# Performance work log

Measured on AMD Instinct MI355X. Metric: run time of the kernel, lower is better.

## Reference

```python
import jax, jax.numpy as jnp
import numpy as np

S, DIM, E, K = 16384, 4096, 64, 2

def setup_inputs() -> dict:
    key = jax.random.key(0)
    kx, kw = jax.random.split(key)
    x = jax.random.normal(kx, (S, DIM), dtype=jnp.float32)
    W = jax.random.normal(kw, (E, DIM), dtype=jnp.float32) * (1.0 / np.sqrt(DIM))
    b = jnp.zeros((E,), dtype=jnp.float32)
    return {"x": x, "W": W, "b": b}

def reference(x, W, b):
    # Router linear: [S, dim] @ [dim, E] + [E] -> [S, E]
    logits = jnp.einsum('sd,ed->se', x, W) + b
    probs = jax.nn.softmax(logits, axis=-1)              # [S, E]
    topk_vals, topk_idx = jax.lax.top_k(probs, K)        # [S, K], [S, K]
    # Load-balance aux loss (Switch Transformer style)
    importance = probs.mean(axis=0)                      # [E]
    hard1 = topk_idx[:, 0]                               # [S]
    load = jax.ops.segment_sum(jnp.ones((S,), dtype=probs.dtype), hard1,
                               num_segments=E) / max(S, 1)
    aux_loss = E * jnp.sum(importance * load)
    return (topk_idx, topk_vals, aux_loss)
```

## Files before the change

### kernel.cpp

```cpp
#include <hip/hip_runtime.h>
#include <hip/hip_bf16.h>

#define SROWS 16384
#define DIMK  4096
#define NE    64
#define BM    16
#define NBLK  (SROWS/BM)
#define KSEG  1024
#define NSTEP 16
#define WSPLIT_SHORTS 262144
#define WSOFF_F 262144
#define WSOFF2  (WSOFF_F + NBLK*64)

typedef __attribute__((ext_vector_type(8))) short short8;
typedef __attribute__((ext_vector_type(4))) float f32x4;

__device__ __forceinline__ void split8(const float4 a, const float4 c, short8& hi, short8& lo) {
    float f[8] = {a.x, a.y, a.z, a.w, c.x, c.y, c.z, c.w};
    #pragma unroll
    for (int i = 0; i < 8; ++i) {
        unsigned short h = __bfloat16_as_ushort(__float2bfloat16(f[i]));
        float hf = __uint_as_float((unsigned)h << 16);
        unsigned short l = __bfloat16_as_ushort(__float2bfloat16(f[i] - hf));
        hi[i] = (short)h;
        lo[i] = (short)l;
    }
}

__global__ void w_split(const float* __restrict__ W, unsigned short* __restrict__ wsp)
{
    const int idx   = blockIdx.x * 256 + threadIdx.x;
    const int kslot = idx & 511;
    const int e     = idx >> 9;
    const float* p = W + (size_t)e * DIMK + kslot * 8;
    float4 va = *reinterpret_cast<const float4*>(p);
    float4 vb = *reinterpret_cast<const float4*>(p + 4);
    short8 hi, lo;
    split8(va, vb, hi, lo);
    *reinterpret_cast<short8*>(wsp + (size_t)(kslot * 64 + e) * 8)                 = hi;
    *reinterpret_cast<short8*>(wsp + WSPLIT_SHORTS + (size_t)(kslot * 64 + e) * 8) = lo;
}

__global__ __launch_bounds__(256, 4) void gate_main(
    const float* __restrict__ x, const unsigned short* __restrict__ wsp,
    const float* __restrict__ b, float* __restrict__ out, float* __restrict__ ws)
{
    __shared__ float smem[4672];
    float* const part = smem;
    float* const Lb   = smem + 3072;
    float* const red  = smem + 4160;

    const int tid  = threadIdx.x;
    const int lane = tid & 63;
    const int ksw  = __builtin_amdgcn_readfirstlane(tid >> 6);
    const int row0 = blockIdx.x * BM;

    const float* xA = x + (size_t)(row0 + (lane & 15)) * DIMK
                        + ksw * KSEG + (lane >> 4) * 8;
    const unsigned short* wBbase = wsp + ((size_t)(ksw * 128) * 64) * 8;

    f32x4 acc[4];
    #pragma unroll
    for (int n = 0; n < 4; ++n) acc[n] = (f32x4){0.f, 0.f, 0.f, 0.f};

    float4 a00 = *reinterpret_cast<const float4*>(xA);
    float4 a01 = *reinterpret_cast<const float4*>(xA + 4);
    float4 a10 = *reinterpret_cast<const float4*>(xA + 32);
    float4 a11 = *reinterpret_cast<const float4*>(xA + 36);

    #pragma unroll 1
    for (int st = 0; st < NSTEP; ++st) {
        const int pst = (st + 1 < NSTEP) ? st + 1 : NSTEP - 1;
        const float* xp = xA + (size_t)pst * 64;
        float4 p00 = *reinterpret_cast<const float4*>(xp);
        float4 p01 = *reinterpret_cast<const float4*>(xp + 4);
        float4 p10 = *reinterpret_cast<const float4*>(xp + 32);
        float4 p11 = *reinterpret_cast<const float4*>(xp + 36);
        __builtin_amdgcn_sched_barrier(0);

        #pragma unroll
        for (int c2 = 0; c2 < 2; ++c2) {
            short8 ah, al;
            if (c2 == 0) split8(a00, a01, ah, al);
            else         split8(a10, a11, ah, al);

            const int ksl = st * 8 + c2 * 4 + (lane >> 4);
            const unsigned short* bp = wBbase + ((size_t)ksl * 64 + (lane & 15)) * 8;
            short8 bh[4], bl[4];
            #pragma unroll
            for (int n = 0; n < 4; ++n) {
                bh[n] = *reinterpret_cast<const short8*>(bp + n * 128);
                bl[n] = *reinterpret_cast<const short8*>(bp + WSPLIT_SHORTS + n * 128);
            }

            #pragma unroll
            for (int n = 0; n < 4; ++n)
                acc[n] = __builtin_amdgcn_mfma_f32_16x16x32_bf16(ah, bh[n], acc[n], 0, 0, 0);
            #pragma unroll
            for (int n = 0; n < 4; ++n)
                acc[n] = __builtin_amdgcn_mfma_f32_16x16x32_bf16(ah, bl[n], acc[n], 0, 0, 0);
            #pragma unroll
            for (int n = 0; n < 4; ++n)
                acc[n] = __builtin_amdgcn_mfma_f32_16x16x32_bf16(al, bh[n], acc[n], 0, 0, 0);
        }

        __builtin_amdgcn_sched_barrier(0);
        a00 = p00; a01 = p01; a10 = p10; a11 = p11;
    }

    __syncthreads();

    if (ksw > 0) {
        #pragma unroll
        for (int n = 0; n < 4; ++n)
            #pragma unroll
            for (int j = 0; j < 4; ++j)
                part[(ksw - 1) * 1024 + lane * 16 + n * 4 + j] = acc[n][j];
    }
    __syncthreads();
    if (ksw == 0) {
        #pragma unroll
        for (int n = 0; n < 4; ++n) {
            #pragma unroll
            for (int j = 0; j < 4; ++j) {
                float v = acc[n][j]
                        + part[0 * 1024 + lane * 16 + n * 4 + j]
                        + part[1 * 1024 + lane * 16 + n * 4 + j]
                        + part[2 * 1024 + lane * 16 + n * 4 + j];
                const int e  = n * 16 + (lane & 15);
                const int rl = (lane >> 4) * 4 + j;
                Lb[e * 17 + rl] = v;
            }
        }
    }
    __syncthreads();

    float impAcc = 0.f, cntAcc = 0.f;
    const float blane = b[lane];
    float* outIdx = out;
    float* outVal = out + (size_t)SROWS * 2;

    #pragma unroll 1
    for (int rr = 0; rr < 4; ++rr) {
        const int r = ksw * 4 + rr;
        const float logit = Lb[lane * 17 + r] + blane;

        float v1 = logit; int i1 = lane;
        #pragma unroll
        for (int off = 32; off; off >>= 1) {
            float ov = __shfl_xor(v1, off);
            int   oi = __shfl_xor(i1, off);
            if (ov > v1 || (ov == v1 && oi < i1)) { v1 = ov; i1 = oi; }
        }
        float p = expf(logit - v1);
        float ssum = p;
        #pragma unroll
        for (int off = 32; off; off >>= 1) ssum += __shfl_xor(ssum, off);

        float v2 = (lane == i1) ? -3.402823466e38f : logit;
        int i2 = lane;
        #pragma unroll
        for (int off = 32; off; off >>= 1) {
            float ov = __shfl_xor(v2, off);
            int   oi = __shfl_xor(i2, off);
            if (ov > v2 || (ov == v2 && oi < i2)) { v2 = ov; i2 = oi; }
        }

        impAcc += p / ssum;
        cntAcc += (i1 == lane) ? 1.f : 0.f;

        if (lane == 0) {
            const int sr = row0 + r;
            outIdx[sr * 2 + 0] = (float)i1;
            outIdx[sr * 2 + 1] = (float)i2;
            outVal[sr * 2 + 0] = 1.f / ssum;
            outVal[sr * 2 + 1] = expf(v2 - v1) / ssum;
        }
    }

    __syncthreads();
    red[ksw * 64 + lane]       = impAcc;
    red[256 + ksw * 64 + lane] = cntAcc;
    __syncthreads();
    if (tid < 64) {
        float si = 0.f, sc2 = 0.f;
        #pragma unroll
        for (int g = 0; g < 4; ++g) {
            si  += red[g * 64 + tid];
            sc2 += red[256 + g * 64 + tid];
        }
        ws[WSOFF_F + (size_t)blockIdx.x * 64 + tid] = si;
        ws[WSOFF2  + (size_t)blockIdx.x * 64 + tid] = sc2;
    }
}

__global__ void gate_reduce(const float* __restrict__ ws, float* __restrict__ out)
{
    __shared__ float li[64 * 64], lc[64 * 64];
    const int t = threadIdx.x;
    const int g  = t >> 4;
    const int e4 = (t & 15) * 4;
    float4 si = make_float4(0.f, 0.f, 0.f, 0.f);
    float4 sc = make_float4(0.f, 0.f, 0.f, 0.f);
    const int base = g * 16;
    #pragma unroll 4
    for (int bb = base; bb < base + 16; ++bb) {
        float4 a = *reinterpret_cast<const float4*>(&ws[WSOFF_F + (size_t)bb * 64 + e4]);
        float4 c = *reinterpret_cast<const float4*>(&ws[WSOFF2  + (size_t)bb * 64 + e4]);
        si.x += a.x; si.y += a.y; si.z += a.z; si.w += a.w;
        sc.x += c.x; sc.y += c.y; sc.z += c.z; sc.w += c.w;
    }
    *reinterpret_cast<float4*>(&li[g * 64 + e4]) = si;
    *reinterpret_cast<float4*>(&lc[g * 64 + e4]) = sc;
    __syncthreads();
    if (t < 64) {
        float ti = 0.f, tc = 0.f;
        #pragma unroll 8
        for (int gg = 0; gg < 64; ++gg) { ti += li[gg * 64 + t]; tc += lc[gg * 64 + t]; }
        li[t] = ti * tc;
    }
    __syncthreads();
    if (t == 0) {
        float s = 0.f;
        for (int i = 0; i < NE; ++i) s += li[i];
        out[(size_t)SROWS * 4] = s * ((float)NE / ((float)SROWS * (float)SROWS));
    }
}

extern "C" void kernel_launch(void* const* d_in, const int* in_sizes, int n_in,
                              void* d_out, int out_size, void* d_ws, size_t ws_size,
                              hipStream_t stream)
{
    const float* x = (const float*)d_in[0];
    const float* W = (const float*)d_in[1];
    const float* b = (const float*)d_in[2];
    float* out = (float*)d_out;
    unsigned short* wsp = (unsigned short*)d_ws;
    float* wsf = (float*)d_ws;

    w_split<<<128, 256, 0, stream>>>(W, wsp);
    gate_main<<<NBLK, 256, 0, stream>>>(x, wsp, b, out, wsf);
    gate_reduce<<<1, 1024, 0, stream>>>(wsf, out);
}
```

Before: 94.89 us.

## Stage split W tiles in LDS via async global-to-LDS loads, 64-row blocks

Raises the rows per block from 16 to 64, using 16 waves (4 row groups by 4 K-splits). The split bf16 hi/lo W tiles are now staged into double-buffered LDS with global_load_lds, so each W fetch is shared across four row groups instead of every wave reading W from global/L2. This cuts redundant W traffic, but adds a per-step barrier and 128KB of dynamic LDS per block, which limits occupancy to one block per CU. The epilogue and the final reduction are resized for 256 blocks.

```diff
diff --git a/kernel.cpp b/kernel.cpp
--- a/kernel.cpp
+++ b/kernel.cpp
@@ -4,13 +4,13 @@
 #define SROWS 16384
 #define DIMK  4096
 #define NE    64
-#define BM    16
+#define BM    64
 #define NBLK  (SROWS/BM)
-#define KSEG  1024
 #define NSTEP 16
 #define WSPLIT_SHORTS 262144
 #define WSOFF_F 262144
 #define WSOFF2  (WSOFF_F + NBLK*64)
+#define LDS_BYTES 131072
 
 typedef __attribute__((ext_vector_type(8))) short short8;
 typedef __attribute__((ext_vector_type(4))) float f32x4;
@@ -41,23 +41,43 @@
     *reinterpret_cast<short8*>(wsp + WSPLIT_SHORTS + (size_t)(kslot * 64 + e) * 8) = lo;
 }
 
-__global__ __launch_bounds__(256, 4) void gate_main(
+__device__ __forceinline__ void gl_lds16(const void* g, void* l) {
+    __builtin_amdgcn_global_load_lds(
+        (const __attribute__((address_space(1))) void*)g,
+        (__attribute__((address_space(3))) void*)l, 16, 0, 0);
+}
+
+__global__ __launch_bounds__(1024, 4) void gate_main(
     const float* __restrict__ x, const unsigned short* __restrict__ wsp,
     const float* __restrict__ b, float* __restrict__ out, float* __restrict__ ws)
 {
-    __shared__ float smem[4672];
-    float* const part = smem;
-    float* const Lb   = smem + 3072;
-    float* const red  = smem + 4160;
+    extern __shared__ __align__(16) char smem[];
 
     const int tid  = threadIdx.x;
     const int lane = tid & 63;
-    const int ksw  = __builtin_amdgcn_readfirstlane(tid >> 6);
+    const int wid  = __builtin_amdgcn_readfirstlane(tid >> 6);
+    const int mw   = wid & 3;
+    const int ksw  = wid >> 2;
     const int row0 = blockIdx.x * BM;
 
-    const float* xA = x + (size_t)(row0 + (lane & 15)) * DIMK
-                        + ksw * KSEG + (lane >> 4) * 8;
-    const unsigned short* wBbase = wsp + ((size_t)(ksw * 128) * 64) * 8;
+    const int spl = tid >> 9;
+    const int skl = (tid >> 6) & 7;
+    const int se  = tid & 63;
+    const unsigned short* bsrc[4];
+    #pragma unroll
+    for (int j = 0; j < 4; ++j)
+        bsrc[j] = wsp + (size_t)spl * WSPLIT_SHORTS
+                + ((size_t)((j * 128 + skl) * 64 + se)) * 8;
+
+    auto STAGE_B = [&](int st, int bsel) {
+        char* Bb = smem + bsel * 65536;
+        #pragma unroll
+        for (int j = 0; j < 4; ++j)
+            gl_lds16(bsrc[j] + (size_t)st * 4096, Bb + j * 16384 + tid * 16);
+    };
+
+    const float* xA = x + (size_t)(row0 + mw * 16 + (lane & 15)) * DIMK
+                        + ksw * 1024 + (lane >> 4) * 8;
 
     f32x4 acc[4];
     #pragma unroll
@@ -67,55 +87,69 @@
     float4 a01 = *reinterpret_cast<const float4*>(xA + 4);
     float4 a10 = *reinterpret_cast<const float4*>(xA + 32);
     float4 a11 = *reinterpret_cast<const float4*>(xA + 36);
+    STAGE_B(0, 0);
+    asm volatile("s_waitcnt vmcnt(0)" ::: "memory");
+    __builtin_amdgcn_s_barrier();
+    __builtin_amdgcn_sched_barrier(0);
+
+    const int kb0 = (lane >> 4) * 1024 + (lane & 15) * 16;
 
     #pragma unroll 1
     for (int st = 0; st < NSTEP; ++st) {
-        const int pst = (st + 1 < NSTEP) ? st + 1 : NSTEP - 1;
-        const float* xp = xA + (size_t)pst * 64;
-        float4 p00 = *reinterpret_cast<const float4*>(xp);
-        float4 p01 = *reinterpret_cast<const float4*>(xp + 4);
-        float4 p10 = *reinterpret_cast<const float4*>(xp + 32);
-        float4 p11 = *reinterpret_cast<const float4*>(xp + 36);
+        float4 p00, p01, p10, p11;
+        const bool hn = (st + 1 < NSTEP);
+        if (hn) {
+            const float* xp = xA + (size_t)(st + 1) * 64;
+            p00 = *reinterpret_cast<const float4*>(xp);
+            p01 = *reinterpret_cast<const float4*>(xp + 4);
+            p10 = *reinterpret_cast<const float4*>(xp + 32);
+            p11 = *reinterpret_cast<const float4*>(xp + 36);
+            STAGE_B(st + 1, (st + 1) & 1);
+        }
         __builtin_amdgcn_sched_barrier(0);
 
-        #pragma unroll
-        for (int c2 = 0; c2 < 2; ++c2) {
-            short8 ah, al;
-            if (c2 == 0) split8(a00, a01, ah, al);
-            else         split8(a10, a11, ah, al);
-
-            const int ksl = st * 8 + c2 * 4 + (lane >> 4);
-            const unsigned short* bp = wBbase + ((size_t)ksl * 64 + (lane & 15)) * 8;
-            short8 bh[4], bl[4];
-            #pragma unroll
-            for (int n = 0; n < 4; ++n) {
-                bh[n] = *reinterpret_cast<const short8*>(bp + n * 128);
-                bl[n] = *reinterpret_cast<const short8*>(bp + WSPLIT_SHORTS + n * 128);
-            }
-
-            #pragma unroll
-            for (int n = 0; n < 4; ++n)
-                acc[n] = __builtin_amdgcn_mfma_f32_16x16x32_bf16(ah, bh[n], acc[n], 0, 0, 0);
-            #pragma unroll
-            for (int n = 0; n < 4; ++n)
-                acc[n] = __builtin_amdgcn_mfma_f32_16x16x32_bf16(ah, bl[n], acc[n], 0, 0, 0);
-            #pragma unroll
-            for (int n = 0; n < 4; ++n)
-                acc[n] = __builtin_amdgcn_mfma_f32_16x16x32_bf16(al, bh[n], acc[n], 0, 0, 0);
-        }
-
+        const char* Bb = smem + (st & 1) * 65536 + ksw * 16384 + kb0;
+
+        short8 ah, al;
+        split8(a00, a01, ah, al);
+        #pragma unroll
+        for (int n = 0; n < 4; ++n) {
+            short8 bh = *reinterpret_cast<const short8*>(Bb + n * 256);
+            short8 bl = *reinterpret_cast<const short8*>(Bb + 8192 + n * 256);
+            acc[n] = __builtin_amdgcn_mfma_f32_16x16x32_bf16(ah, bh, acc[n], 0, 0, 0);
+            acc[n] = __builtin_amdgcn_mfma_f32_16x16x32_bf16(ah, bl, acc[n], 0, 0, 0);
+            acc[n] = __builtin_amdgcn_mfma_f32_16x16x32_bf16(al, bh, acc[n], 0, 0, 0);
+        }
+
+        split8(a10, a11, ah, al);
+        #pragma unroll
+        for (int n = 0; n < 4; ++n) {
+            short8 bh = *reinterpret_cast<const short8*>(Bb + 4096 + n * 256);
+            short8 bl = *reinterpret_cast<const short8*>(Bb + 4096 + 8192 + n * 256);
+            acc[n] = __builtin_amdgcn_mfma_f32_16x16x32_bf16(ah, bh, acc[n], 0, 0, 0);
+            acc[n] = __builtin_amdgcn_mfma_f32_16x16x32_bf16(ah, bl, acc[n], 0, 0, 0);
+            acc[n] = __builtin_amdgcn_mfma_f32_16x16x32_bf16(al, bh, acc[n], 0, 0, 0);
+        }
+
+        asm volatile("s_waitcnt vmcnt(0)" ::: "memory");
+        __builtin_amdgcn_s_barrier();
         __builtin_amdgcn_sched_barrier(0);
-        a00 = p00; a01 = p01; a10 = p10; a11 = p11;
-    }
-
-    __syncthreads();
+        if (hn) { a00 = p00; a01 = p01; a10 = p10; a11 = p11; }
+    }
+
+    __syncthreads();
+
+    float* const part = reinterpret_cast<float*>(smem);
+    float* const Lb   = reinterpret_cast<float*>(smem + 49152);
+    float* const red  = reinterpret_cast<float*>(smem + 66048);
 
     if (ksw > 0) {
+        const int base = ((ksw - 1) * 4 + mw) * 1024 + lane * 16;
         #pragma unroll
         for (int n = 0; n < 4; ++n)
             #pragma unroll
             for (int j = 0; j < 4; ++j)
-                part[(ksw - 1) * 1024 + lane * 16 + n * 4 + j] = acc[n][j];
+                part[base + n * 4 + j] = acc[n][j];
     }
     __syncthreads();
     if (ksw == 0) {
@@ -124,12 +158,12 @@
             #pragma unroll
             for (int j = 0; j < 4; ++j) {
                 float v = acc[n][j]
-                        + part[0 * 1024 + lane * 16 + n * 4 + j]
-                        + part[1 * 1024 + lane * 16 + n * 4 + j]
-                        + part[2 * 1024 + lane * 16 + n * 4 + j];
+                        + part[(0 * 4 + mw) * 1024 + lane * 16 + n * 4 + j]
+                        + part[(1 * 4 + mw) * 1024 + lane * 16 + n * 4 + j]
+                        + part[(2 * 4 + mw) * 1024 + lane * 16 + n * 4 + j];
                 const int e  = n * 16 + (lane & 15);
-                const int rl = (lane >> 4) * 4 + j;
-                Lb[e * 17 + rl] = v;
+                const int rl = mw * 16 + (lane >> 4) * 4 + j;
+                Lb[e * 65 + rl] = v;
             }
         }
     }
@@ -142,8 +176,8 @@
 
     #pragma unroll 1
     for (int rr = 0; rr < 4; ++rr) {
-        const int r = ksw * 4 + rr;
-        const float logit = Lb[lane * 17 + r] + blane;
+        const int r = wid * 4 + rr;
+        const float logit = Lb[lane * 65 + r] + blane;
 
         float v1 = logit; int i1 = lane;
         #pragma unroll
@@ -179,15 +213,15 @@
     }
 
     __syncthreads();
-    red[ksw * 64 + lane]       = impAcc;
-    red[256 + ksw * 64 + lane] = cntAcc;
+    red[wid * 64 + lane]        = impAcc;
+    red[1024 + wid * 64 + lane] = cntAcc;
     __syncthreads();
     if (tid < 64) {
         float si = 0.f, sc2 = 0.f;
         #pragma unroll
-        for (int g = 0; g < 4; ++g) {
+        for (int g = 0; g < 16; ++g) {
             si  += red[g * 64 + tid];
-            sc2 += red[256 + g * 64 + tid];
+            sc2 += red[1024 + g * 64 + tid];
         }
         ws[WSOFF_F + (size_t)blockIdx.x * 64 + tid] = si;
         ws[WSOFF2  + (size_t)blockIdx.x * 64 + tid] = sc2;
@@ -202,9 +236,9 @@
     const int e4 = (t & 15) * 4;
     float4 si = make_float4(0.f, 0.f, 0.f, 0.f);
     float4 sc = make_float4(0.f, 0.f, 0.f, 0.f);
-    const int base = g * 16;
-    #pragma unroll 4
-    for (int bb = base; bb < base + 16; ++bb) {
+    const int base = g * 4;
+    #pragma unroll
+    for (int bb = base; bb < base + 4; ++bb) {
         float4 a = *reinterpret_cast<const float4*>(&ws[WSOFF_F + (size_t)bb * 64 + e4]);
         float4 c = *reinterpret_cast<const float4*>(&ws[WSOFF2  + (size_t)bb * 64 + e4]);
         si.x += a.x; si.y += a.y; si.z += a.z; si.w += a.w;
@@ -238,7 +272,10 @@
     unsigned short* wsp = (unsigned short*)d_ws;
     float* wsf = (float*)d_ws;
 
+    hipFuncSetAttribute(reinterpret_cast<const void*>(gate_main),
+                        hipFuncAttributeMaxDynamicSharedMemorySize, LDS_BYTES);
+
     w_split<<<128, 256, 0, stream>>>(W, wsp);
-    gate_main<<<NBLK, 256, 0, stream>>>(x, wsp, b, out, wsf);
+    gate_main<<<NBLK, 1024, LDS_BYTES, stream>>>(x, wsp, b, out, wsf);
     gate_reduce<<<1, 1024, 0, stream>>>(wsf, out);
 }
```

Result: faster. 82.02 us (-13.6%).
